# Optimization experiments

Measured on AMD Instinct MI355X. Metric: run time of the kernel, lower is better.

Reference implementation:

```python
import jax, jax.numpy as jnp
import numpy as np


def setup_inputs() -> dict:
    key = jax.random.key(0)
    k0, k1 = jax.random.split(key)
    B, S, T = 32, 512, 128
    return {
        "crf_score_0": jax.random.normal(k0, (B, S + 1, T, T), dtype=jnp.float32),
        "crf_score_1": jax.random.normal(k1, (B, S + 1, T), dtype=jnp.float32),
        "sof": 126,
        "eof": 127,
    }


def reference(crf_score_0, crf_score_1, sof, eof):
    # crf_score_0: [B, S+1, T, T], crf_score_1: [B, S+1, T]
    # Initial scores (note: original multiplies, not adds, at step 0)
    forscores = crf_score_0[:, 0, sof, :] * crf_score_1[:, 0, :]  # [B, T]

    # Move seq axis first for scan: [S, B, T, T] and [S, B, T]
    c0 = jnp.moveaxis(crf_score_0[:, 1:], 0, 1)
    c1 = jnp.moveaxis(crf_score_1[:, 1:], 0, 1)

    def fwd_step(fs, xs):
        t0, t1 = xs  # [B, T, T], [B, T]
        # cur[b, i, j] = fs[b, i] + t1[b, j] + t0[b, i, j]
        cur = fs[:, :, None] + t1[:, None, :] + t0
        new_fs = jnp.max(cur, axis=1)            # [B, T]
        bp = jnp.argmax(cur, axis=1).astype(jnp.int32)  # [B, T]
        return new_fs, bp

    _, back_points = jax.lax.scan(fwd_step, forscores, (c0, c1))  # bps: [S, B, T]

    # Backtrack exactly as the original loop: pointer starts at bp[-1][:, eof],
    # then for idx = S-1 .. 0: pointer = bp[idx][b, pointer]; decode[:, idx] = pointer.
    ptr0 = back_points[-1][:, eof]  # [B]

    def bwd_step(ptr, bp_t):
        new = jnp.take_along_axis(bp_t, ptr[:, None], axis=1)[:, 0]
        return new, new

    _, dec = jax.lax.scan(bwd_step, ptr0, back_points, reverse=True)  # [S, B]
    return dec.T.astype(jnp.int32)  # [B, S] decoded label indices
```

## Files before the change

kernel.cpp:

```cpp
#include <hip/hip_runtime.h>


constexpr int S = 512;
constexpr int T = 128;

__global__ __launch_bounds__(1024, 1)
void viterbi_fused(const float* __restrict__ c0, const float* __restrict__ c1,
                   const int* __restrict__ sofp, const int* __restrict__ eofp,
                   int* __restrict__ out)
{
    __shared__ float fs[2][T];
    __shared__ float pmax[32][T];
    __shared__ int   parg[32][T];
    __shared__ unsigned char bp[S][T];

    const int b   = blockIdx.x;
    const int tid = (int)threadIdx.x;
    const int jq  = tid & 31;
    const int g   = tid >> 5;
    const int col = jq * 4;
    const int row = g * 4;

    const float* c0b = c0 + (size_t)b * (S + 1) * T * T;
    const float* c1b = c1 + (size_t)b * (S + 1) * T;

    if (tid < T) {
        const int sof = sofp[0];
        fs[0][tid] = c0b[(size_t)sof * T + tid] * c1b[tid];
    }
    __syncthreads();

    {
    }
    const float* t0p = c0b + (size_t)1 * T * T;
    const float* t1p = c1b + (size_t)1 * T;
    float4 a0 = *(const float4*)(t0p + (size_t)(row + 0) * T + col);
    float4 a1 = *(const float4*)(t0p + (size_t)(row + 1) * T + col);
    float4 a2 = *(const float4*)(t0p + (size_t)(row + 2) * T + col);
    float4 a3 = *(const float4*)(t0p + (size_t)(row + 3) * T + col);
    float4 tv = *(const float4*)(t1p + col);

    int p = 0;
    for (int s = 1; s <= S; ++s) {
        float4 b0 = make_float4(0.f,0.f,0.f,0.f), b1 = b0, b2 = b0, b3 = b0, bt = b0;
        if (s < S) {
            const float* n0 = c0b + (size_t)(s + 1) * T * T;
            const float* n1 = c1b + (size_t)(s + 1) * T;
            b0 = *(const float4*)(n0 + (size_t)(row + 0) * T + col);
            b1 = *(const float4*)(n0 + (size_t)(row + 1) * T + col);
            b2 = *(const float4*)(n0 + (size_t)(row + 2) * T + col);
            b3 = *(const float4*)(n0 + (size_t)(row + 3) * T + col);
            bt = *(const float4*)(n1 + col);
        }

        const float f0 = fs[p][row + 0];
        const float f1 = fs[p][row + 1];
        const float f2 = fs[p][row + 2];
        const float f3 = fs[p][row + 3];

        float bx, by, bz, bw; int ix, iy, iz, iw; float v;
        bx = (f0 + tv.x) + a0.x; ix = row;
        by = (f0 + tv.y) + a0.y; iy = row;
        bz = (f0 + tv.z) + a0.z; iz = row;
        bw = (f0 + tv.w) + a0.w; iw = row;

        v = (f1 + tv.x) + a1.x; if (v > bx) { bx = v; ix = row + 1; }
        v = (f1 + tv.y) + a1.y; if (v > by) { by = v; iy = row + 1; }
        v = (f1 + tv.z) + a1.z; if (v > bz) { bz = v; iz = row + 1; }
        v = (f1 + tv.w) + a1.w; if (v > bw) { bw = v; iw = row + 1; }

        v = (f2 + tv.x) + a2.x; if (v > bx) { bx = v; ix = row + 2; }
        v = (f2 + tv.y) + a2.y; if (v > by) { by = v; iy = row + 2; }
        v = (f2 + tv.z) + a2.z; if (v > bz) { bz = v; iz = row + 2; }
        v = (f2 + tv.w) + a2.w; if (v > bw) { bw = v; iw = row + 2; }

        v = (f3 + tv.x) + a3.x; if (v > bx) { bx = v; ix = row + 3; }
        v = (f3 + tv.y) + a3.y; if (v > by) { by = v; iy = row + 3; }
        v = (f3 + tv.z) + a3.z; if (v > bz) { bz = v; iz = row + 3; }
        v = (f3 + tv.w) + a3.w; if (v > bw) { bw = v; iw = row + 3; }

        *(float4*)&pmax[g][col] = make_float4(bx, by, bz, bw);
        *(int4*)  &parg[g][col] = make_int4(ix, iy, iz, iw);
        __syncthreads();

        if (tid < T) {
            float bb = pmax[0][tid];
            int   ii = parg[0][tid];
            #pragma unroll
            for (int gg = 1; gg < 32; ++gg) {
                float vv = pmax[gg][tid];
                if (vv > bb) { bb = vv; ii = parg[gg][tid]; }
            }
            fs[p ^ 1][tid] = bb;
            bp[s - 1][tid] = (unsigned char)ii;
        }
        __syncthreads();

        p ^= 1;
        a0 = b0; a1 = b1; a2 = b2; a3 = b3; tv = bt;
    }

    if (tid == 0) {
        const int eof = eofp[0];
        int ptr = bp[S - 1][eof];
        for (int idx = S - 1; idx >= 0; --idx) {
            ptr = bp[idx][ptr];
            out[(size_t)b * S + idx] = ptr;
        }
    }
}

extern "C" void kernel_launch(void* const* d_in, const int* in_sizes, int n_in,
                              void* d_out, int out_size, void* d_ws, size_t ws_size,
                              hipStream_t stream)
{
    const float* c0  = (const float*)d_in[0];
    const float* c1  = (const float*)d_in[1];
    const int*   sof = (const int*)d_in[2];
    const int*   eof = (const int*)d_in[3];
    int*         out = (int*)d_out;

    const int B = in_sizes[1] / ((S + 1) * T);
    viterbi_fused<<<dim3(B), dim3(1024), 0, stream>>>(c0, c1, sof, eof, out);
}
```

Baseline: 849.4 us.

## Split each batch's Viterbi forward across 16 cooperating workgroups with atomic handoff

```diff
diff --git a/kernel.cpp b/kernel.cpp
--- a/kernel.cpp
+++ b/kernel.cpp
@@ -1,18 +1,195 @@
 #include <hip/hip_runtime.h>
 
 
-constexpr int S = 512;
-constexpr int T = 128;
+constexpr int S    = 512;
+constexpr int T    = 128;
+constexpr int NSL  = 16;
+constexpr int ROWS = T / NSL;
+
+using u64 = unsigned long long;
+using u32 = unsigned int;
+
+__device__ __forceinline__ u32 flipf(u32 u) {
+    return u ^ (0x80000000u | (u32)((int)u >> 31));
+}
+__device__ __forceinline__ u32 unflipf(u32 y) {
+    return y ^ (0x80000000u | ~(u32)((int)y >> 31));
+}
+
+__global__ __launch_bounds__(128, 1)
+void viterbi_fwd(const float* __restrict__ c0, const float* __restrict__ c1,
+                 const int* __restrict__ sofp,
+                 u64* __restrict__ pub,
+                 unsigned char* __restrict__ bp)
+{
+    __shared__ float fs_lds[ROWS];
+    __shared__ int   seq_lds;
+
+    const int g    = blockIdx.x;
+    const int b    = g & 31;
+    const int k    = g >> 5;
+    const int tid  = (int)threadIdx.x;
+    const int wv   = tid >> 6;
+    const int l    = tid & 63;
+    const int row0 = k * ROWS;
+
+    const float* c0b = c0 + (size_t)b * (S + 1) * T * T;
+    const float* c1b = c1 + (size_t)b * (S + 1) * T;
+    u64* pubB = pub + (size_t)b * 2 * NSL * T;
+
+    if (wv == 0) {
+        if (l == 0) seq_lds = 0;
+
+        const int rA   = 2 * (l >> 4);
+        const int cB   = (l & 15) * 8;
+        const u32 tieA = (u32)(127 - (row0 + rA));
+        const u32 tieB = (u32)(127 - (row0 + rA + 1));
+
+        const int sof = sofp[0];
+        float f0 = c0b[(size_t)sof * T + row0 + rA]     * c1b[row0 + rA];
+        float f1 = c0b[(size_t)sof * T + row0 + rA + 1] * c1b[row0 + rA + 1];
+
+        const float* pA = c0b + (size_t)T * T + (size_t)(row0 + rA) * T + cB;
+        const float* qA = c1b + T + cB;
+        const float* pB = pA + T * T;
+        const float* qB = qA + T;
+
+        float4 A00 = *(const float4*)(pA);
+        float4 A01 = *(const float4*)(pA + 4);
+        float4 A10 = *(const float4*)(pA + T);
+        float4 A11 = *(const float4*)(pA + T + 4);
+        float4 At0 = *(const float4*)(qA);
+        float4 At1 = *(const float4*)(qA + 4);
+        float4 B00 = *(const float4*)(pB);
+        float4 B01 = *(const float4*)(pB + 4);
+        float4 B10 = *(const float4*)(pB + T);
+        float4 B11 = *(const float4*)(pB + T + 4);
+        float4 Bt0 = *(const float4*)(qB);
+        float4 Bt1 = *(const float4*)(qB + 4);
+
+        auto STEP = [&](int s, float4& x00, float4& x01, float4& x10,
+                        float4& x11, float4& xt0, float4& xt1,
+                        const float*& pp, const float*& qq) {
+            const u32 sTag = (u32)s << 8;
+            const u32 loA  = sTag | tieA;
+            const u32 loB  = sTag | tieB;
+
+            auto mk = [&](float a0c, float a1c, float t1c) -> u64 {
+                float vA = (f0 + t1c) + a0c;
+                float vB = (f1 + t1c) + a1c;
+                bool  t  = vB > vA;
+                u32 hi = flipf(__float_as_uint(t ? vB : vA));
+                u32 lo = t ? loB : loA;
+                return ((u64)hi << 32) | lo;
+            };
+            u64 k0 = mk(x00.x, x10.x, xt0.x);
+            u64 k1 = mk(x00.y, x10.y, xt0.y);
+            u64 k2 = mk(x00.z, x10.z, xt0.z);
+            u64 k3 = mk(x00.w, x10.w, xt0.w);
+            u64 k4 = mk(x01.x, x11.x, xt1.x);
+            u64 k5 = mk(x01.y, x11.y, xt1.y);
+            u64 k6 = mk(x01.z, x11.z, xt1.z);
+            u64 k7 = mk(x01.w, x11.w, xt1.w);
+
+            if (s + 2 <= S) {
+                pp += 2 * T * T;
+                qq += 2 * T;
+                x00 = *(const float4*)(pp);
+                x01 = *(const float4*)(pp + 4);
+                x10 = *(const float4*)(pp + T);
+                x11 = *(const float4*)(pp + T + 4);
+                xt0 = *(const float4*)(qq);
+                xt1 = *(const float4*)(qq + 4);
+            }
+
+            auto red = [&](u64& kk) {
+                u64 p16 = __shfl_xor(kk, 16, 64); if (p16 > kk) kk = p16;
+                u64 p32 = __shfl_xor(kk, 32, 64); if (p32 > kk) kk = p32;
+            };
+            red(k0); red(k1); red(k2); red(k3);
+            red(k4); red(k5); red(k6); red(k7);
+
+            u64 ka = (rA == 0) ? k0 : (rA == 2) ? k2 : (rA == 4) ? k4 : k6;
+            u64 kb = (rA == 0) ? k1 : (rA == 2) ? k3 : (rA == 4) ? k5 : k7;
+            u64* ps = pubB + (size_t)(s & 1) * NSL * T + (size_t)k * T + cB + rA;
+            __hip_atomic_store(ps,     ka, __ATOMIC_RELAXED, __HIP_MEMORY_SCOPE_AGENT);
+            __hip_atomic_store(ps + 1, kb, __ATOMIC_RELAXED, __HIP_MEMORY_SCOPE_AGENT);
+
+            while (__hip_atomic_load(&seq_lds, __ATOMIC_ACQUIRE,
+                                     __HIP_MEMORY_SCOPE_WORKGROUP) != s) {}
+            float2 fp = *(const float2*)&fs_lds[rA];
+            f0 = fp.x;
+            f1 = fp.y;
+        };
+
+        for (int s = 1; s <= S; s += 2) {
+            STEP(s,     A00, A01, A10, A11, At0, At1, pA, qA);
+            STEP(s + 1, B00, B01, B10, B11, Bt0, Bt1, pB, qB);
+        }
+    } else {
+        const int row = l & 7;
+        const int slq = (l >> 3) * 2;
+        const size_t joff = (size_t)(row0 + row);
+
+        for (int s = 1; s <= S; ++s) {
+            const u64* p0 = pubB + (size_t)(s & 1) * NSL * T +
+                            (size_t)slq * T + joff;
+            u64 v0, v1;
+            for (;;) {
+                v0 = __hip_atomic_load(p0,     __ATOMIC_RELAXED, __HIP_MEMORY_SCOPE_AGENT);
+                v1 = __hip_atomic_load(p0 + T, __ATOMIC_RELAXED, __HIP_MEMORY_SCOPE_AGENT);
+                bool ok = (((u32)v0 >> 8) == (u32)s) && (((u32)v1 >> 8) == (u32)s);
+                if (__all(ok)) break;
+            }
+            u64 m = (v1 > v0) ? v1 : v0;
+            { u64 p = __shfl_xor(m, 8,  64); if (p > m) m = p; }
+            { u64 p = __shfl_xor(m, 16, 64); if (p > m) m = p; }
+            { u64 p = __shfl_xor(m, 32, 64); if (p > m) m = p; }
+            if (l < 8) {
+                float val = __uint_as_float(unflipf((u32)(m >> 32)));
+                int   ii  = 127 - (int)((u32)m & 0xffu);
+                fs_lds[l] = val;
+                bp[((size_t)b * S + (s - 1)) * T + row0 + l] = (unsigned char)ii;
+            }
+            if (l == 0)
+                __hip_atomic_store(&seq_lds, s, __ATOMIC_RELEASE,
+                                   __HIP_MEMORY_SCOPE_WORKGROUP);
+        }
+    }
+}
 
 __global__ __launch_bounds__(1024, 1)
-void viterbi_fused(const float* __restrict__ c0, const float* __restrict__ c1,
-                   const int* __restrict__ sofp, const int* __restrict__ eofp,
-                   int* __restrict__ out)
+void viterbi_bwd(const unsigned char* __restrict__ bp,
+                 const int* __restrict__ eofp, int* __restrict__ out)
+{
+    __shared__ unsigned char lbp[S][T];
+    const int b   = blockIdx.x;
+    const int tid = (int)threadIdx.x;
+
+    const uint4* s4 = (const uint4*)(bp + (size_t)b * S * T);
+    uint4* d4 = (uint4*)&lbp[0][0];
+    #pragma unroll
+    for (int it = 0; it < 4; ++it) d4[tid + it * 1024] = s4[tid + it * 1024];
+    __syncthreads();
+
+    if (tid == 0) {
+        int ptr = lbp[S - 1][eofp[0]];
+        for (int idx = S - 1; idx >= 0; --idx) {
+            ptr = lbp[idx][ptr];
+            out[(size_t)b * S + idx] = ptr;
+        }
+    }
+}
+
+__global__ __launch_bounds__(1024, 1)
+void viterbi_fused_fb(const float* __restrict__ c0, const float* __restrict__ c1,
+                      const int* __restrict__ sofp, const int* __restrict__ eofp,
+                      int* __restrict__ out)
 {
     __shared__ float fs[2][T];
     __shared__ float pmax[32][T];
     __shared__ int   parg[32][T];
-    __shared__ unsigned char bp[S][T];
+    __shared__ unsigned char bpl[S][T];
 
     const int b   = blockIdx.x;
     const int tid = (int)threadIdx.x;
@@ -30,29 +207,24 @@
     }
     __syncthreads();
 
-    {
-    }
-    const float* t0p = c0b + (size_t)1 * T * T;
-    const float* t1p = c1b + (size_t)1 * T;
+    const float* t0p = c0b + (size_t)T * T;
     float4 a0 = *(const float4*)(t0p + (size_t)(row + 0) * T + col);
     float4 a1 = *(const float4*)(t0p + (size_t)(row + 1) * T + col);
     float4 a2 = *(const float4*)(t0p + (size_t)(row + 2) * T + col);
     float4 a3 = *(const float4*)(t0p + (size_t)(row + 3) * T + col);
-    float4 tv = *(const float4*)(t1p + col);
+    float4 tv = *(const float4*)(c1b + T + col);
 
     int p = 0;
     for (int s = 1; s <= S; ++s) {
         float4 b0 = make_float4(0.f,0.f,0.f,0.f), b1 = b0, b2 = b0, b3 = b0, bt = b0;
         if (s < S) {
             const float* n0 = c0b + (size_t)(s + 1) * T * T;
-            const float* n1 = c1b + (size_t)(s + 1) * T;
             b0 = *(const float4*)(n0 + (size_t)(row + 0) * T + col);
             b1 = *(const float4*)(n0 + (size_t)(row + 1) * T + col);
             b2 = *(const float4*)(n0 + (size_t)(row + 2) * T + col);
             b3 = *(const float4*)(n0 + (size_t)(row + 3) * T + col);
-            bt = *(const float4*)(n1 + col);
-        }
-
+            bt = *(const float4*)(c1b + (size_t)(s + 1) * T + col);
+        }
         const float f0 = fs[p][row + 0];
         const float f1 = fs[p][row + 1];
         const float f2 = fs[p][row + 2];
@@ -63,17 +235,14 @@
         by = (f0 + tv.y) + a0.y; iy = row;
         bz = (f0 + tv.z) + a0.z; iz = row;
         bw = (f0 + tv.w) + a0.w; iw = row;
-
         v = (f1 + tv.x) + a1.x; if (v > bx) { bx = v; ix = row + 1; }
         v = (f1 + tv.y) + a1.y; if (v > by) { by = v; iy = row + 1; }
         v = (f1 + tv.z) + a1.z; if (v > bz) { bz = v; iz = row + 1; }
         v = (f1 + tv.w) + a1.w; if (v > bw) { bw = v; iw = row + 1; }
-
         v = (f2 + tv.x) + a2.x; if (v > bx) { bx = v; ix = row + 2; }
         v = (f2 + tv.y) + a2.y; if (v > by) { by = v; iy = row + 2; }
         v = (f2 + tv.z) + a2.z; if (v > bz) { bz = v; iz = row + 2; }
         v = (f2 + tv.w) + a2.w; if (v > bw) { bw = v; iw = row + 2; }
-
         v = (f3 + tv.x) + a3.x; if (v > bx) { bx = v; ix = row + 3; }
         v = (f3 + tv.y) + a3.y; if (v > by) { by = v; iy = row + 3; }
         v = (f3 + tv.z) + a3.z; if (v > bz) { bz = v; iz = row + 3; }
@@ -92,19 +261,18 @@
                 if (vv > bb) { bb = vv; ii = parg[gg][tid]; }
             }
             fs[p ^ 1][tid] = bb;
-            bp[s - 1][tid] = (unsigned char)ii;
+            bpl[s - 1][tid] = (unsigned char)ii;
         }
         __syncthreads();
-
         p ^= 1;
         a0 = b0; a1 = b1; a2 = b2; a3 = b3; tv = bt;
     }
 
     if (tid == 0) {
         const int eof = eofp[0];
-        int ptr = bp[S - 1][eof];
+        int ptr = bpl[S - 1][eof];
         for (int idx = S - 1; idx >= 0; --idx) {
-            ptr = bp[idx][ptr];
+            ptr = bpl[idx][ptr];
             out[(size_t)b * S + idx] = ptr;
         }
     }
@@ -121,5 +289,15 @@
     int*         out = (int*)d_out;
 
     const int B = in_sizes[1] / ((S + 1) * T);
-    viterbi_fused<<<dim3(B), dim3(1024), 0, stream>>>(c0, c1, sof, eof, out);
-}
+
+    const size_t pub_bytes = (size_t)B * 2 * NSL * T * 8;
+    const size_t bp_bytes  = (size_t)B * S * T;
+    if (ws_size >= pub_bytes + bp_bytes) {
+        u64* pub = (u64*)d_ws;
+        unsigned char* bp = (unsigned char*)d_ws + pub_bytes;
+        viterbi_fwd<<<dim3(B * NSL), dim3(128), 0, stream>>>(c0, c1, sof, pub, bp);
+        viterbi_bwd<<<dim3(B), dim3(1024), 0, stream>>>(bp, eof, out);
+    } else {
+        viterbi_fused_fb<<<dim3(B), dim3(1024), 0, stream>>>(c0, c1, sof, eof, out);
+    }
+}
```

Measured after the change: 1.276 ms. 1.5x slower.

## Split each batch's Viterbi forward pass across eight cooperating workgroups

Applied to the files above, without the earlier changes.

```diff
diff --git a/kernel.cpp b/kernel.cpp
--- a/kernel.cpp
+++ b/kernel.cpp
@@ -1,25 +1,248 @@
 #include <hip/hip_runtime.h>
 
 
-constexpr int S = 512;
-constexpr int T = 128;
+constexpr int S   = 512;
+constexpr int T   = 128;
+constexpr int NSL = 8;
+constexpr int RW  = 16;
+constexpr int NW  = S / 2;
+
+using u64 = unsigned long long;
+using u32 = unsigned int;
+
+__device__ __forceinline__ void bar_lds() {
+    asm volatile("s_waitcnt lgkmcnt(0)" ::: "memory");
+    __builtin_amdgcn_s_barrier();
+}
+__device__ __forceinline__ u32 flipf(u32 u)   { return u ^ (0x80000000u | (u32)((int)u >> 31)); }
+__device__ __forceinline__ u32 unflipf(u32 y) { return y ^ (0x80000000u | ~(u32)((int)y >> 31)); }
+__device__ __forceinline__ u64 aload(const u64* p) {
+    return __hip_atomic_load(p, __ATOMIC_RELAXED, __HIP_MEMORY_SCOPE_AGENT);
+}
+__device__ __forceinline__ void astore(u64* p, u64 v) {
+    __hip_atomic_store(p, v, __ATOMIC_RELAXED, __HIP_MEMORY_SCOPE_AGENT);
+}
+
+#define GLDS(srcp, dstp) \
+    __builtin_amdgcn_global_load_lds( \
+        (const __attribute__((address_space(1))) void*)(srcp), \
+        (__attribute__((address_space(3))) void*)(dstp), 16, 0, 0)
+
+__global__ __launch_bounds__(512, 1)
+void viterbi_fwd2(const float* __restrict__ c0, const float* __restrict__ c1,
+                  const int* __restrict__ sofp,
+                  u64* __restrict__ pubG, u64* __restrict__ pubH,
+                  unsigned char* __restrict__ bp)
+{
+    __shared__ float t0b_lds[2][T * T];
+    __shared__ float t0a_lds[RW * T];
+    __shared__ float part_v[16 * 130];
+    __shared__ unsigned char part_j[16 * 132];
+    __shared__ float gaval[T];
+    __shared__ float fs_lds[RW];
+    __shared__ u64   pollH[128];
+    __shared__ u64   pollG[128];
+
+    const int g    = blockIdx.x;
+    const int b    = g & 31;
+    const int k    = g >> 5;
+    const int tid  = (int)threadIdx.x;
+    const int wv   = tid >> 6;
+    const int lane = tid & 63;
+
+    const float* c0b = c0 + (size_t)b * (S + 1) * T * T;
+    const float* c1b = c1 + (size_t)b * (S + 1) * T;
+    u64* pG = pubG + (size_t)b * 2 * NSL * T;
+    u64* pH = pubH + (size_t)b * 2 * NSL * T;
+
+    const int jA  = tid >> 2;
+    const int ihA = tid & 3;
+    const int jh  = tid >> 5;
+    const int mq  = tid & 31;
+
+    auto STAGE = [&](int w) {
+        if (wv < 4) return;
+        const int fo = (wv - 4) * 256 + lane * 4;
+        const float* srcB = c0b + (size_t)(2 * w + 2) * T * T + fo;
+        float* dstB = &t0b_lds[w & 1][(wv - 4) * 256];
+        #pragma unroll
+        for (int q = 0; q < 16; ++q)
+            GLDS(srcB + q * 1024, dstB + q * 1024);
+        const float* srcA = c0b + (size_t)(2 * w + 1) * T * T
+                          + (size_t)k * RW * T + fo;
+        float* dstA = &t0a_lds[(wv - 4) * 256];
+        #pragma unroll
+        for (int q = 0; q < 2; ++q)
+            GLDS(srcA + q * 1024, dstA + q * 1024);
+    };
+
+    STAGE(0);
+    float  t1a_s = c1b[(size_t)1 * T + jA];
+    float4 t1b_s = *(const float4*)&c1b[(size_t)2 * T + mq * 4];
+    if (tid < RW) {
+        const int sof = sofp[0];
+        fs_lds[tid] = c0b[(size_t)sof * T + k * RW + tid] * c1b[k * RW + tid];
+    }
+    asm volatile("s_waitcnt vmcnt(0)" ::: "memory");
+    bar_lds();
+
+    for (int w = 0; w < NW; ++w) {
+        const u32 tagw = (u32)(w + 1);
+
+        {
+            float bv; int bi;
+            {
+                float f = fs_lds[ihA * 4 + 0];
+                bv = (f + t1a_s) + t0a_lds[(ihA * 4 + 0) * T + jA];
+                bi = ihA * 4 + 0;
+            }
+            #pragma unroll
+            for (int d = 1; d < 4; ++d) {
+                float f = fs_lds[ihA * 4 + d];
+                float v = (f + t1a_s) + t0a_lds[(ihA * 4 + d) * T + jA];
+                if (v > bv) { bv = v; bi = ihA * 4 + d; }
+            }
+            u64 kk = ((u64)flipf(__float_as_uint(bv)) << 32)
+                   | ((u32)(127 - (k * RW + bi)) << 24) | tagw;
+            u64 p1 = __shfl_xor(kk, 1, 64); if (p1 > kk) kk = p1;
+            u64 p2 = __shfl_xor(kk, 2, 64); if (p2 > kk) kk = p2;
+            if (ihA == 0) {
+                astore(&pG[(size_t)(w & 1) * NSL * T + (size_t)k * T + jA], kk);
+                gaval[jA] = __uint_as_float(unflipf((u32)(kk >> 32)));
+            }
+        }
+        bar_lds();
+
+        {
+            const float4 ga0 = *(const float4*)&gaval[jh * 8];
+            const float4 ga1 = *(const float4*)&gaval[jh * 8 + 4];
+            const float* tb = &t0b_lds[w & 1][0];
+            float bv0, bv1, bv2, bv3; int bj0, bj1, bj2, bj3;
+            {
+                const int j = jh * 8;
+                float4 t0 = *(const float4*)&tb[j * T + mq * 4];
+                bv0 = (ga0.x + t1b_s.x) + t0.x;
+                bv1 = (ga0.x + t1b_s.y) + t0.y;
+                bv2 = (ga0.x + t1b_s.z) + t0.z;
+                bv3 = (ga0.x + t1b_s.w) + t0.w;
+                bj0 = bj1 = bj2 = bj3 = j;
+            }
+            const float gs[8] = {ga0.x, ga0.y, ga0.z, ga0.w, ga1.x, ga1.y, ga1.z, ga1.w};
+            #pragma unroll
+            for (int jj = 1; jj < 8; ++jj) {
+                const int j = jh * 8 + jj;
+                const float gg = gs[jj];
+                float4 t0 = *(const float4*)&tb[j * T + mq * 4];
+                float v;
+                v = (gg + t1b_s.x) + t0.x; if (v > bv0) { bv0 = v; bj0 = j; }
+                v = (gg + t1b_s.y) + t0.y; if (v > bv1) { bv1 = v; bj1 = j; }
+                v = (gg + t1b_s.z) + t0.z; if (v > bv2) { bv2 = v; bj2 = j; }
+                v = (gg + t1b_s.w) + t0.w; if (v > bv3) { bv3 = v; bj3 = j; }
+            }
+            *(float4*)&part_v[jh * 130 + mq * 4] = make_float4(bv0, bv1, bv2, bv3);
+            *(u32*)&part_j[jh * 132 + mq * 4] =
+                (u32)bj0 | ((u32)bj1 << 8) | ((u32)bj2 << 16) | ((u32)bj3 << 24);
+        }
+        bar_lds();
+
+        if (tid < 128) {
+            float bv = part_v[tid]; int bt = 0;
+            #pragma unroll
+            for (int t = 1; t < 16; ++t) {
+                float v = part_v[t * 130 + tid];
+                if (v > bv) { bv = v; bt = t; }
+            }
+            u32 j = part_j[bt * 132 + tid];
+            astore(&pH[(size_t)(w & 1) * NSL * T + (size_t)k * T + tid],
+                   ((u64)flipf(__float_as_uint(bv)) << 32) | ((127u - j) << 24) | tagw);
+        }
+        if (w + 1 < NW) STAGE(w + 1);
+        float  t1a_n = t1a_s;
+        float4 t1b_n = t1b_s;
+        if (w + 1 < NW) {
+            t1a_n = c1b[(size_t)(2 * w + 3) * T + jA];
+            t1b_n = *(const float4*)&c1b[(size_t)(2 * w + 4) * T + mq * 4];
+        }
+
+        if (tid < 128) {
+            const u64* p = &pH[(size_t)(w & 1) * NSL * T + (size_t)(tid & 7) * T
+                               + (k * RW + (tid >> 3))];
+            u64 v;
+            do { v = aload(p); } while ((u32)(v & 0xFFFFFFu) != tagw);
+            pollH[tid] = v;
+        } else if (tid < 256) {
+            const int t2 = tid - 128;
+            const u64* p = &pG[(size_t)(w & 1) * NSL * T + (size_t)(t2 & 7) * T
+                               + (k * RW + (t2 >> 3))];
+            u64 v;
+            do { v = aload(p); } while ((u32)(v & 0xFFFFFFu) != tagw);
+            pollG[t2] = v;
+        } else {
+            asm volatile("s_waitcnt vmcnt(0)" ::: "memory");
+        }
+        bar_lds();
+
+        if (tid < 16) {
+            u64 mh = pollH[tid * 8];
+            #pragma unroll
+            for (int t = 1; t < 8; ++t) { u64 c = pollH[tid * 8 + t]; if (c > mh) mh = c; }
+            fs_lds[tid] = __uint_as_float(unflipf((u32)(mh >> 32)));
+            bp[((size_t)b * S + (2 * w + 1)) * T + (k * RW + tid)] =
+                (unsigned char)(127u - (((u32)mh >> 24) & 0xFFu));
+        } else if (tid < 32) {
+            const int t2 = tid - 16;
+            u64 mg = pollG[t2 * 8];
+            #pragma unroll
+            for (int t = 1; t < 8; ++t) { u64 c = pollG[t2 * 8 + t]; if (c > mg) mg = c; }
+            bp[((size_t)b * S + (2 * w)) * T + (k * RW + t2)] =
+                (unsigned char)(127u - (((u32)mg >> 24) & 0xFFu));
+        }
+        bar_lds();
+
+        t1a_s = t1a_n;
+        t1b_s = t1b_n;
+    }
+}
 
 __global__ __launch_bounds__(1024, 1)
-void viterbi_fused(const float* __restrict__ c0, const float* __restrict__ c1,
-                   const int* __restrict__ sofp, const int* __restrict__ eofp,
-                   int* __restrict__ out)
+void viterbi_bwd(const unsigned char* __restrict__ bp,
+                 const int* __restrict__ eofp, int* __restrict__ out)
+{
+    __shared__ unsigned char lbp[S][T];
+    const int b   = blockIdx.x;
+    const int tid = (int)threadIdx.x;
+
+    const uint4* s4 = (const uint4*)(bp + (size_t)b * S * T);
+    uint4* d4 = (uint4*)&lbp[0][0];
+    #pragma unroll
+    for (int it = 0; it < 4; ++it) d4[tid + it * 1024] = s4[tid + it * 1024];
+    __syncthreads();
+
+    if (tid == 0) {
+        int ptr = lbp[S - 1][eofp[0]];
+        for (int idx = S - 1; idx >= 0; --idx) {
+            ptr = lbp[idx][ptr];
+            out[(size_t)b * S + idx] = ptr;
+        }
+    }
+}
+
+__global__ __launch_bounds__(1024, 1)
+void viterbi_fused_fb(const float* __restrict__ c0, const float* __restrict__ c1,
+                      const int* __restrict__ sofp, const int* __restrict__ eofp,
+                      int* __restrict__ out)
 {
     __shared__ float fs[2][T];
     __shared__ float pmax[32][T];
     __shared__ int   parg[32][T];
-    __shared__ unsigned char bp[S][T];
+    __shared__ unsigned char bpl[S][T];
 
     const int b   = blockIdx.x;
     const int tid = (int)threadIdx.x;
     const int jq  = tid & 31;
-    const int g   = tid >> 5;
+    const int gg2 = tid >> 5;
     const int col = jq * 4;
-    const int row = g * 4;
+    const int row = gg2 * 4;
 
     const float* c0b = c0 + (size_t)b * (S + 1) * T * T;
     const float* c1b = c1 + (size_t)b * (S + 1) * T;
@@ -30,29 +253,24 @@
     }
     __syncthreads();
 
-    {
-    }
-    const float* t0p = c0b + (size_t)1 * T * T;
-    const float* t1p = c1b + (size_t)1 * T;
+    const float* t0p = c0b + (size_t)T * T;
     float4 a0 = *(const float4*)(t0p + (size_t)(row + 0) * T + col);
     float4 a1 = *(const float4*)(t0p + (size_t)(row + 1) * T + col);
     float4 a2 = *(const float4*)(t0p + (size_t)(row + 2) * T + col);
     float4 a3 = *(const float4*)(t0p + (size_t)(row + 3) * T + col);
-    float4 tv = *(const float4*)(t1p + col);
+    float4 tv = *(const float4*)(c1b + T + col);
 
     int p = 0;
     for (int s = 1; s <= S; ++s) {
         float4 b0 = make_float4(0.f,0.f,0.f,0.f), b1 = b0, b2 = b0, b3 = b0, bt = b0;
         if (s < S) {
             const float* n0 = c0b + (size_t)(s + 1) * T * T;
-            const float* n1 = c1b + (size_t)(s + 1) * T;
             b0 = *(const float4*)(n0 + (size_t)(row + 0) * T + col);
             b1 = *(const float4*)(n0 + (size_t)(row + 1) * T + col);
             b2 = *(const float4*)(n0 + (size_t)(row + 2) * T + col);
             b3 = *(const float4*)(n0 + (size_t)(row + 3) * T + col);
-            bt = *(const float4*)(n1 + col);
-        }
-
+            bt = *(const float4*)(c1b + (size_t)(s + 1) * T + col);
+        }
         const float f0 = fs[p][row + 0];
         const float f1 = fs[p][row + 1];
         const float f2 = fs[p][row + 2];
@@ -63,48 +281,44 @@
         by = (f0 + tv.y) + a0.y; iy = row;
         bz = (f0 + tv.z) + a0.z; iz = row;
         bw = (f0 + tv.w) + a0.w; iw = row;
-
         v = (f1 + tv.x) + a1.x; if (v > bx) { bx = v; ix = row + 1; }
         v = (f1 + tv.y) + a1.y; if (v > by) { by = v; iy = row + 1; }
         v = (f1 + tv.z) + a1.z; if (v > bz) { bz = v; iz = row + 1; }
         v = (f1 + tv.w) + a1.w; if (v > bw) { bw = v; iw = row + 1; }
-
         v = (f2 + tv.x) + a2.x; if (v > bx) { bx = v; ix = row + 2; }
         v = (f2 + tv.y) + a2.y; if (v > by) { by = v; iy = row + 2; }
         v = (f2 + tv.z) + a2.z; if (v > bz) { bz = v; iz = row + 2; }
         v = (f2 + tv.w) + a2.w; if (v > bw) { bw = v; iw = row + 2; }
-
         v = (f3 + tv.x) + a3.x; if (v > bx) { bx = v; ix = row + 3; }
         v = (f3 + tv.y) + a3.y; if (v > by) { by = v; iy = row + 3; }
         v = (f3 + tv.z) + a3.z; if (v > bz) { bz = v; iz = row + 3; }
         v = (f3 + tv.w) + a3.w; if (v > bw) { bw = v; iw = row + 3; }
 
-        *(float4*)&pmax[g][col] = make_float4(bx, by, bz, bw);
-        *(int4*)  &parg[g][col] = make_int4(ix, iy, iz, iw);
+        *(float4*)&pmax[gg2][col] = make_float4(bx, by, bz, bw);
+        *(int4*)  &parg[gg2][col] = make_int4(ix, iy, iz, iw);
         __syncthreads();
 
         if (tid < T) {
             float bb = pmax[0][tid];
             int   ii = parg[0][tid];
             #pragma unroll
-            for (int gg = 1; gg < 32; ++gg) {
-                float vv = pmax[gg][tid];
-                if (vv > bb) { bb = vv; ii = parg[gg][tid]; }
+            for (int q = 1; q < 32; ++q) {
+                float vv = pmax[q][tid];
+                if (vv > bb) { bb = vv; ii = parg[q][tid]; }
             }
             fs[p ^ 1][tid] = bb;
-            bp[s - 1][tid] = (unsigned char)ii;
+            bpl[s - 1][tid] = (unsigned char)ii;
         }
         __syncthreads();
-
         p ^= 1;
         a0 = b0; a1 = b1; a2 = b2; a3 = b3; tv = bt;
     }
 
     if (tid == 0) {
         const int eof = eofp[0];
-        int ptr = bp[S - 1][eof];
+        int ptr = bpl[S - 1][eof];
         for (int idx = S - 1; idx >= 0; --idx) {
-            ptr = bp[idx][ptr];
+            ptr = bpl[idx][ptr];
             out[(size_t)b * S + idx] = ptr;
         }
     }
@@ -121,5 +335,16 @@
     int*         out = (int*)d_out;
 
     const int B = in_sizes[1] / ((S + 1) * T);
-    viterbi_fused<<<dim3(B), dim3(1024), 0, stream>>>(c0, c1, sof, eof, out);
-}
+
+    const size_t pub_b = (size_t)B * 2 * NSL * T * 8;
+    const size_t bp_b  = (size_t)B * S * T;
+    if (B == 32 && ws_size >= 2 * pub_b + bp_b) {
+        u64* pubG = (u64*)d_ws;
+        u64* pubH = (u64*)((char*)d_ws + pub_b);
+        unsigned char* bp = (unsigned char*)d_ws + 2 * pub_b;
+        viterbi_fwd2<<<dim3(B * NSL), dim3(512), 0, stream>>>(c0, c1, sof, pubG, pubH, bp);
+        viterbi_bwd<<<dim3(B), dim3(1024), 0, stream>>>(bp, eof, out);
+    } else {
+        viterbi_fused_fb<<<dim3(B), dim3(1024), 0, stream>>>(c0, c1, sof, eof, out);
+    }
+}
```

Result: faster. 817.9 us (-3.7%).

## Split each Viterbi chain across 8 blocks with global-memory flag publishing

Applied to the files above, without the earlier changes.

```diff
diff --git a/kernel.cpp b/kernel.cpp
--- a/kernel.cpp
+++ b/kernel.cpp
@@ -1,25 +1,223 @@
 #include <hip/hip_runtime.h>
 
 
-constexpr int S = 512;
-constexpr int T = 128;
+constexpr int S   = 512;
+constexpr int T   = 128;
+constexpr int NSL = 8;
+constexpr int NQ  = 8;
+constexpr int C   = 4;
+
+using u64 = unsigned long long;
+using u32 = unsigned int;
+
+__device__ __forceinline__ void bar_lds() {
+    asm volatile("s_waitcnt lgkmcnt(0)" ::: "memory");
+    __builtin_amdgcn_s_barrier();
+}
+__device__ __forceinline__ u32 flipf(u32 u)   { return u ^ (0x80000000u | (u32)((int)u >> 31)); }
+__device__ __forceinline__ u32 unflipf(u32 y) { return y ^ (0x80000000u | ~(u32)((int)y >> 31)); }
+__device__ __forceinline__ u64 aload(const u64* p) {
+    return __hip_atomic_load(p, __ATOMIC_RELAXED, __HIP_MEMORY_SCOPE_AGENT);
+}
+__device__ __forceinline__ void astore(u64* p, u64 v) {
+    __hip_atomic_store(p, v, __ATOMIC_RELAXED, __HIP_MEMORY_SCOPE_AGENT);
+}
+
+__global__ __launch_bounds__(384, 1)
+void viterbi_fwd4(const float* __restrict__ c0, const float* __restrict__ c1,
+                  const int* __restrict__ sofp,
+                  u64* __restrict__ pub,
+                  unsigned char* __restrict__ bp)
+{
+    __shared__ float fs_lds[2][C][16];
+
+    const int g   = blockIdx.x;
+    const int k   = g >> 3;
+    const int q   = g & 7;
+    const int tid = (int)threadIdx.x;
+    const int wv  = tid >> 6;
+    const int ln  = tid & 63;
+
+    if (tid < C * 16) {
+        const int c  = tid >> 4;
+        const int lr = tid & 15;
+        const int b  = q + NQ * c;
+        const float* c0b = c0 + (size_t)b * (S + 1) * T * T;
+        const float* c1b = c1 + (size_t)b * (S + 1) * T;
+        const int sof = sofp[0];
+        fs_lds[0][c][lr] = c0b[(size_t)sof * T + k * 16 + lr] * c1b[k * 16 + lr];
+    }
+    bar_lds();
+
+    if (wv < 4) {
+        const int rr   = (ln >> 3) & 7;
+        const int cc   = ln & 7;
+        const int col0 = wv * 32 + cc * 4;
+        const int iA   = k * 16 + 2 * rr;
+        const u32 tie24A = (u32)(127 - iA) << 24;
+
+        const float* c0b[1]; (void)c0b;
+        #define DECL_CHAIN(c)                                                   \
+            const float* c0b##c = c0 + (size_t)(q + NQ * c) * (S + 1) * T * T;  \
+            const float* c1b##c = c1 + (size_t)(q + NQ * c) * (S + 1) * T;      \
+            const float* pA##c = c0b##c + (size_t)T * T + (size_t)iA * T + col0;\
+            const float* qA##c = c1b##c + T + col0;                             \
+            const float* pB##c = pA##c + T * T;                                 \
+            const float* qB##c = qA##c + T;                                     \
+            float4 A0##c = *(const float4*)(pA##c);                             \
+            float4 A1##c = *(const float4*)(pA##c + T);                         \
+            float4 At##c = *(const float4*)(qA##c);                             \
+            float4 B0##c = *(const float4*)(pB##c);                             \
+            float4 B1##c = *(const float4*)(pB##c + T);                         \
+            float4 Bt##c = *(const float4*)(qB##c);                             \
+            u64* pub##c = pub + (size_t)(q + NQ * c) * 2 * NSL * T;
+        DECL_CHAIN(0) DECL_CHAIN(1) DECL_CHAIN(2) DECL_CHAIN(3)
+        #undef DECL_CHAIN
+
+        auto CSTEP = [&](int s, int par, const float* fsP,
+                         const float*& pp, const float*& qq,
+                         float4& R0, float4& R1, float4& T1, u64* pubC) {
+            float2 f = *(const float2*)&fsP[2 * rr];
+            const u32 loA = tie24A | (u32)s;
+            const u32 loB = loA - (1u << 24);
+            auto mk = [&](float a0, float a1, float t1c) -> u64 {
+                float vA = (f.x + t1c) + a0;
+                float vB = (f.y + t1c) + a1;
+                bool  t  = vB > vA;
+                return ((u64)flipf(__float_as_uint(t ? vB : vA)) << 32)
+                     | (t ? loB : loA);
+            };
+            u64 k0 = mk(R0.x, R1.x, T1.x);
+            u64 k1 = mk(R0.y, R1.y, T1.y);
+            u64 k2 = mk(R0.z, R1.z, T1.z);
+            u64 k3 = mk(R0.w, R1.w, T1.w);
+
+            if (s + 2 <= S) {
+                pp += 2 * T * T;
+                qq += 2 * T;
+                R0 = *(const float4*)(pp);
+                R1 = *(const float4*)(pp + T);
+                T1 = *(const float4*)(qq);
+            }
+
+            auto red = [&](u64& kk) {
+                u64 p;
+                p = __shfl_xor(kk, 8,  64); if (p > kk) kk = p;
+                p = __shfl_xor(kk, 16, 64); if (p > kk) kk = p;
+                p = __shfl_xor(kk, 32, 64); if (p > kk) kk = p;
+            };
+            red(k0); red(k1); red(k2); red(k3);
+
+            if (rr == 0) {
+                u64* slot = pubC + ((size_t)par * NSL + k) * T + col0;
+                astore(slot + 0, k0);
+                astore(slot + 1, k1);
+                astore(slot + 2, k2);
+                astore(slot + 3, k3);
+            }
+        };
+
+        for (int s = 1; s <= S; s += 2) {
+            {
+                const float* fsP = &fs_lds[(s + 1) & 1][0][0];
+                CSTEP(s, s & 1, fsP + 0,  pA0, qA0, A00, A10, At0, pub0);
+                CSTEP(s, s & 1, fsP + 16, pA1, qA1, A01, A11, At1, pub1);
+                CSTEP(s, s & 1, fsP + 32, pA2, qA2, A02, A12, At2, pub2);
+                CSTEP(s, s & 1, fsP + 48, pA3, qA3, A03, A13, At3, pub3);
+            }
+            bar_lds();
+            {
+                const float* fsP = &fs_lds[s & 1][0][0];
+                CSTEP(s + 1, (s + 1) & 1, fsP + 0,  pB0, qB0, B00, B10, Bt0, pub0);
+                CSTEP(s + 1, (s + 1) & 1, fsP + 16, pB1, qB1, B01, B11, Bt1, pub1);
+                CSTEP(s + 1, (s + 1) & 1, fsP + 32, pB2, qB2, B02, B12, Bt2, pub2);
+                CSTEP(s + 1, (s + 1) & 1, fsP + 48, pB3, qB3, B03, B13, Bt3, pub3);
+            }
+            bar_lds();
+        }
+    } else {
+        const int pw = wv - 4;
+        const int lr = ln >> 3;
+        const int sl = ln & 7;
+
+        auto POLL = [&](int s, int par, int c) {
+            const int b = q + NQ * c;
+            const u64* base = pub + (size_t)b * 2 * NSL * T
+                            + ((size_t)par * NSL + sl) * T + (k * 16 + lr);
+            u64 v0, v1;
+            for (;;) {
+                v0 = aload(base);
+                v1 = aload(base + 8);
+                bool ok = ((u32)(v0 & 0xFFFFFFu) == (u32)s) &&
+                          ((u32)(v1 & 0xFFFFFFu) == (u32)s);
+                if (__all(ok)) break;
+            }
+            auto red = [&](u64& kk) {
+                u64 p;
+                p = __shfl_xor(kk, 1, 64); if (p > kk) kk = p;
+                p = __shfl_xor(kk, 2, 64); if (p > kk) kk = p;
+                p = __shfl_xor(kk, 4, 64); if (p > kk) kk = p;
+            };
+            red(v0); red(v1);
+            if (sl == 0) {
+                fs_lds[par][c][lr]     = __uint_as_float(unflipf((u32)(v0 >> 32)));
+                fs_lds[par][c][lr + 8] = __uint_as_float(unflipf((u32)(v1 >> 32)));
+                unsigned char* bpr = bp + ((size_t)b * S + (s - 1)) * T + k * 16;
+                bpr[lr]     = (unsigned char)(127u - (((u32)(v0 >> 24)) & 0xFFu));
+                bpr[lr + 8] = (unsigned char)(127u - (((u32)(v1 >> 24)) & 0xFFu));
+            }
+        };
+
+        for (int s = 1; s <= S; s += 2) {
+            POLL(s, s & 1, 2 * pw);
+            POLL(s, s & 1, 2 * pw + 1);
+            bar_lds();
+            POLL(s + 1, (s + 1) & 1, 2 * pw);
+            POLL(s + 1, (s + 1) & 1, 2 * pw + 1);
+            bar_lds();
+        }
+    }
+}
 
 __global__ __launch_bounds__(1024, 1)
-void viterbi_fused(const float* __restrict__ c0, const float* __restrict__ c1,
-                   const int* __restrict__ sofp, const int* __restrict__ eofp,
-                   int* __restrict__ out)
+void viterbi_bwd(const unsigned char* __restrict__ bp,
+                 const int* __restrict__ eofp, int* __restrict__ out)
+{
+    __shared__ unsigned char lbp[S][T];
+    const int b   = blockIdx.x;
+    const int tid = (int)threadIdx.x;
+
+    const uint4* s4 = (const uint4*)(bp + (size_t)b * S * T);
+    uint4* d4 = (uint4*)&lbp[0][0];
+    #pragma unroll
+    for (int it = 0; it < 4; ++it) d4[tid + it * 1024] = s4[tid + it * 1024];
+    __syncthreads();
+
+    if (tid == 0) {
+        int ptr = lbp[S - 1][eofp[0]];
+        for (int idx = S - 1; idx >= 0; --idx) {
+            ptr = lbp[idx][ptr];
+            out[(size_t)b * S + idx] = ptr;
+        }
+    }
+}
+
+__global__ __launch_bounds__(1024, 1)
+void viterbi_fused_fb(const float* __restrict__ c0, const float* __restrict__ c1,
+                      const int* __restrict__ sofp, const int* __restrict__ eofp,
+                      int* __restrict__ out)
 {
     __shared__ float fs[2][T];
     __shared__ float pmax[32][T];
     __shared__ int   parg[32][T];
-    __shared__ unsigned char bp[S][T];
+    __shared__ unsigned char bpl[S][T];
 
     const int b   = blockIdx.x;
     const int tid = (int)threadIdx.x;
     const int jq  = tid & 31;
-    const int g   = tid >> 5;
+    const int gg2 = tid >> 5;
     const int col = jq * 4;
-    const int row = g * 4;
+    const int row = gg2 * 4;
 
     const float* c0b = c0 + (size_t)b * (S + 1) * T * T;
     const float* c1b = c1 + (size_t)b * (S + 1) * T;
@@ -30,29 +228,24 @@
     }
     __syncthreads();
 
-    {
-    }
-    const float* t0p = c0b + (size_t)1 * T * T;
-    const float* t1p = c1b + (size_t)1 * T;
+    const float* t0p = c0b + (size_t)T * T;
     float4 a0 = *(const float4*)(t0p + (size_t)(row + 0) * T + col);
     float4 a1 = *(const float4*)(t0p + (size_t)(row + 1) * T + col);
     float4 a2 = *(const float4*)(t0p + (size_t)(row + 2) * T + col);
     float4 a3 = *(const float4*)(t0p + (size_t)(row + 3) * T + col);
-    float4 tv = *(const float4*)(t1p + col);
+    float4 tv = *(const float4*)(c1b + T + col);
 
     int p = 0;
     for (int s = 1; s <= S; ++s) {
         float4 b0 = make_float4(0.f,0.f,0.f,0.f), b1 = b0, b2 = b0, b3 = b0, bt = b0;
         if (s < S) {
             const float* n0 = c0b + (size_t)(s + 1) * T * T;
-            const float* n1 = c1b + (size_t)(s + 1) * T;
             b0 = *(const float4*)(n0 + (size_t)(row + 0) * T + col);
             b1 = *(const float4*)(n0 + (size_t)(row + 1) * T + col);
             b2 = *(const float4*)(n0 + (size_t)(row + 2) * T + col);
             b3 = *(const float4*)(n0 + (size_t)(row + 3) * T + col);
-            bt = *(const float4*)(n1 + col);
-        }
-
+            bt = *(const float4*)(c1b + (size_t)(s + 1) * T + col);
+        }
         const float f0 = fs[p][row + 0];
         const float f1 = fs[p][row + 1];
         const float f2 = fs[p][row + 2];
@@ -63,48 +256,44 @@
         by = (f0 + tv.y) + a0.y; iy = row;
         bz = (f0 + tv.z) + a0.z; iz = row;
         bw = (f0 + tv.w) + a0.w; iw = row;
-
         v = (f1 + tv.x) + a1.x; if (v > bx) { bx = v; ix = row + 1; }
         v = (f1 + tv.y) + a1.y; if (v > by) { by = v; iy = row + 1; }
         v = (f1 + tv.z) + a1.z; if (v > bz) { bz = v; iz = row + 1; }
         v = (f1 + tv.w) + a1.w; if (v > bw) { bw = v; iw = row + 1; }
-
         v = (f2 + tv.x) + a2.x; if (v > bx) { bx = v; ix = row + 2; }
         v = (f2 + tv.y) + a2.y; if (v > by) { by = v; iy = row + 2; }
         v = (f2 + tv.z) + a2.z; if (v > bz) { bz = v; iz = row + 2; }
         v = (f2 + tv.w) + a2.w; if (v > bw) { bw = v; iw = row + 2; }
-
         v = (f3 + tv.x) + a3.x; if (v > bx) { bx = v; ix = row + 3; }
         v = (f3 + tv.y) + a3.y; if (v > by) { by = v; iy = row + 3; }
         v = (f3 + tv.z) + a3.z; if (v > bz) { bz = v; iz = row + 3; }
         v = (f3 + tv.w) + a3.w; if (v > bw) { bw = v; iw = row + 3; }
 
-        *(float4*)&pmax[g][col] = make_float4(bx, by, bz, bw);
-        *(int4*)  &parg[g][col] = make_int4(ix, iy, iz, iw);
+        *(float4*)&pmax[gg2][col] = make_float4(bx, by, bz, bw);
+        *(int4*)  &parg[gg2][col] = make_int4(ix, iy, iz, iw);
         __syncthreads();
 
         if (tid < T) {
             float bb = pmax[0][tid];
             int   ii = parg[0][tid];
             #pragma unroll
-            for (int gg = 1; gg < 32; ++gg) {
-                float vv = pmax[gg][tid];
-                if (vv > bb) { bb = vv; ii = parg[gg][tid]; }
+            for (int qq2 = 1; qq2 < 32; ++qq2) {
+                float vv = pmax[qq2][tid];
+                if (vv > bb) { bb = vv; ii = parg[qq2][tid]; }
             }
             fs[p ^ 1][tid] = bb;
-            bp[s - 1][tid] = (unsigned char)ii;
+            bpl[s - 1][tid] = (unsigned char)ii;
         }
         __syncthreads();
-
         p ^= 1;
         a0 = b0; a1 = b1; a2 = b2; a3 = b3; tv = bt;
     }
 
     if (tid == 0) {
         const int eof = eofp[0];
-        int ptr = bp[S - 1][eof];
+        int ptr = bpl[S - 1][eof];
         for (int idx = S - 1; idx >= 0; --idx) {
-            ptr = bp[idx][ptr];
+            ptr = bpl[idx][ptr];
             out[(size_t)b * S + idx] = ptr;
         }
     }
@@ -121,5 +310,15 @@
     int*         out = (int*)d_out;
 
     const int B = in_sizes[1] / ((S + 1) * T);
-    viterbi_fused<<<dim3(B), dim3(1024), 0, stream>>>(c0, c1, sof, eof, out);
-}
+
+    const size_t pub_b = (size_t)B * 2 * NSL * T * 8;
+    const size_t bp_b  = (size_t)B * S * T;
+    if (B == 32 && ws_size >= pub_b + bp_b) {
+        u64* pubw = (u64*)d_ws;
+        unsigned char* bpw = (unsigned char*)d_ws + pub_b;
+        viterbi_fwd4<<<dim3(NSL * NQ), dim3(384), 0, stream>>>(c0, c1, sof, pubw, bpw);
+        viterbi_bwd<<<dim3(B), dim3(1024), 0, stream>>>(bpw, eof, out);
+    } else {
+        viterbi_fused_fb<<<dim3(B), dim3(1024), 0, stream>>>(c0, c1, sof, eof, out);
+    }
+}
```

Measured after the change: 1.935 ms. 128% more time.
